# Optimization experiments

Measured on AMD Instinct MI355X. Metric: run time of the kernel, lower is better.

The kernel has to match this reference:

```python
import jax, jax.numpy as jnp
import numpy as np

LAM = 0.1
EPS = 1e-5

def _conv(x, w, b, pad):
    y = jax.lax.conv_general_dilated(x, w, (1, 1), [(pad, pad), (pad, pad)],
                                     dimension_numbers=('NCHW', 'OIHW', 'NCHW'))
    return y + b[None, :, None, None]

def _bn(x, g, b, m, v):
    return (x - m[None, :, None, None]) * (g / jnp.sqrt(v + EPS))[None, :, None, None] + b[None, :, None, None]

def _simam(x):
    # leave-one-out mean/var per HxW map, closed-form single-pass (same math as the
    # original per-pixel mask loop: torch unbiased var over the n-1 'other' values)
    n = x.shape[-2] * x.shape[-1]
    s = jnp.sum(x, axis=(-2, -1), keepdims=True)
    ss = jnp.sum(x * x, axis=(-2, -1), keepdims=True)
    mu = (s - x) / (n - 1)
    var = (ss - x * x - (n - 1) * mu * mu) / (n - 2)
    e = 4.0 * (var + LAM) / ((x - mu) ** 2 + 2.0 * var + 2.0 * LAM)
    return jax.nn.sigmoid(1.0 / e) * x

def setup_inputs():
    B, T, D, H, NC = 128, 128, 64, 256, 5
    IN = 64 * D
    ks = iter(jax.random.split(jax.random.key(0), 64))
    def w(shape, s=0.05):
        return jax.random.normal(next(ks), shape, jnp.float32) * s
    d = {'x': jax.random.normal(next(ks), (B, T, D), jnp.float32)}
    for nm, ci, co, k in [('c1a', 1, 32, 1), ('c1b', 32, 32, 3), ('c2a', 32, 64, 1), ('c2b', 64, 64, 3)]:
        d[nm + '_w'] = w((co, ci, k, k)); d[nm + '_b'] = w((co,))
        bn = 'bn' + nm[1:]
        d[bn + '_g'] = jnp.ones((co,), jnp.float32)
        d[bn + '_b'] = jnp.zeros((co,), jnp.float32)
        d[bn + '_m'] = w((co,), 0.01)
        d[bn + '_v'] = jnp.ones((co,), jnp.float32)
    for i in range(3):
        d['q%d_w' % i] = w((IN, H)); d['q%d_b' % i] = w((IN,))
        d['r%d_w' % i] = w((H, IN)); d['r%d_b' % i] = w((H,))
    d['wih'] = w((4 * H, IN)); d['whh'] = w((4 * H, H))
    d['bih'] = w((4 * H,)); d['bhh'] = w((4 * H,))
    d['fc_w'] = w((NC, H)); d['fc_b'] = w((NC,))
    return d

def reference(x, c1a_w, c1a_b, bn1a_g, bn1a_b, bn1a_m, bn1a_v, c1b_w, c1b_b, bn1b_g, bn1b_b, bn1b_m, bn1b_v, c2a_w, c2a_b, bn2a_g, bn2a_b, bn2a_m, bn2a_v, c2b_w, c2b_b, bn2b_g, bn2b_b, bn2b_m, bn2b_v, q0_w, q0_b, r0_w, r0_b, q1_w, q1_b, r1_w, r1_b, q2_w, q2_b, r2_w, r2_b, wih, whh, bih, bhh, fc_w, fc_b):
    B, T, D = x.shape
    h4 = x[:, None]  # [B,1,T,D]
    h4 = jax.nn.relu(_bn(_conv(h4, c1a_w, c1a_b, 0), bn1a_g, bn1a_b, bn1a_m, bn1a_v))
    h4 = jax.nn.relu(_bn(_conv(h4, c1b_w, c1b_b, 1), bn1b_g, bn1b_b, bn1b_m, bn1b_v))
    h4 = _simam(h4)
    h4 = jax.nn.relu(_bn(_conv(h4, c2a_w, c2a_b, 0), bn2a_g, bn2a_b, bn2a_m, bn2a_v))
    h4 = jax.nn.relu(_bn(_conv(h4, c2b_w, c2b_b, 1), bn2b_g, bn2b_b, bn2b_m, bn2b_v))
    h4 = _simam(h4)
    C = h4.shape[1]
    xl = h4.reshape(B, T, C * D)  # raw reshape, matches torch .view on [B,C,T,D]
    H = whh.shape[1]

    def step(carry, xt):
        h, c = carry
        xm, hm = xt, h
        xm = 2.0 * jax.nn.sigmoid(hm @ q0_w.T + q0_b) * xm  # round 1
        hm = 2.0 * jax.nn.sigmoid(xm @ r0_w.T + r0_b) * hm  # round 2
        xm = 2.0 * jax.nn.sigmoid(hm @ q1_w.T + q1_b) * xm  # round 3
        hm = 2.0 * jax.nn.sigmoid(xm @ r1_w.T + r1_b) * hm  # round 4
        xm = 2.0 * jax.nn.sigmoid(hm @ q2_w.T + q2_b) * xm  # round 5
        hm = 2.0 * jax.nn.sigmoid(xm @ r2_w.T + r2_b) * hm  # round 6
        gates = xm @ wih.T + bih + hm @ whh.T + bhh
        i, f, g, o = jnp.split(gates, 4, axis=-1)  # torch LSTMCell gate order
        c_new = jax.nn.sigmoid(f) * c + jax.nn.sigmoid(i) * jnp.tanh(g)
        h_new = jax.nn.sigmoid(o) * jnp.tanh(c_new)
        return (h_new, c_new), None

    h0 = jnp.zeros((B, H), x.dtype)
    c0 = jnp.zeros((B, H), x.dtype)
    (hT, _), _ = jax.lax.scan(step, (h0, c0), jnp.swapaxes(xl, 0, 1))
    return hT @ fc_w.T + fc_b
```

## Files before the change

kernel.cpp:

```cpp
#include <hip/hip_runtime.h>
#include <math.h>


typedef unsigned short u16;

#define EPSBN 1e-5f

__device__ __forceinline__ float sigf(float x) { return 1.0f / (1.0f + expf(-x)); }

__device__ __forceinline__ float b2f(u16 u) {
  union { unsigned int i; float f; } v; v.i = ((unsigned int)u) << 16; return v.f;
}
__device__ __forceinline__ u16 f2b(float f) {
  union { float f; unsigned int i; } v; v.f = f;
  unsigned int r = v.i + 0x7FFFu + ((v.i >> 16) & 1u);
  return (u16)(r >> 16);
}

template <typename T> __device__ __forceinline__ float ld1(const T* p);
template <> __device__ __forceinline__ float ld1<float>(const float* p) { return *p; }
template <> __device__ __forceinline__ float ld1<u16>(const u16* p) { return b2f(*p); }
template <typename T> __device__ __forceinline__ void st1(T* p, float v);
template <> __device__ __forceinline__ void st1<float>(float* p, float v) { *p = v; }
template <> __device__ __forceinline__ void st1<u16>(u16* p, float v) { *p = f2b(v); }

__device__ __forceinline__ float simam_elem(float xv, float s, float ss) {
  float mu = (s - xv) * (1.0f / 8191.0f);
  float var = (ss - xv * xv - 8191.0f * mu * mu) * (1.0f / 8190.0f);
  float einv = ((xv - mu) * (xv - mu) + 2.0f * var + 0.2f) / (4.0f * (var + 0.1f));
  return xv * sigf(einv);
}

__global__ __launch_bounds__(256) void k_conv1(
    const float* __restrict__ x,
    const float* __restrict__ w1a, const float* __restrict__ b1a,
    const float* __restrict__ g1a, const float* __restrict__ bb1a,
    const float* __restrict__ m1a, const float* __restrict__ v1a,
    const float* __restrict__ w1b, const float* __restrict__ b1b,
    const float* __restrict__ g1b, const float* __restrict__ bb1b,
    const float* __restrict__ m1b, const float* __restrict__ v1b,
    u16* __restrict__ y1u, float* __restrict__ ps1, float* __restrict__ pss1)
{
  __shared__ float xs[6][66];
  __shared__ float a1[32][6][66];
  __shared__ float A1[32], T1[32], S2[32], T2[32];
  __shared__ float reds[4][32], redq[4][32];
  const int tid = threadIdx.x;
  const int b = blockIdx.x, t0 = blockIdx.y * 4;
  if (tid < 32) {
    float s = g1a[tid] * rsqrtf(v1a[tid] + EPSBN);
    A1[tid] = w1a[tid] * s;
    T1[tid] = (b1a[tid] - m1a[tid]) * s + bb1a[tid];
    float s2 = g1b[tid] * rsqrtf(v1b[tid] + EPSBN);
    S2[tid] = s2;
    T2[tid] = (b1b[tid] - m1b[tid]) * s2 + bb1b[tid];
  }
  for (int i = tid; i < 6 * 66; i += 256) {
    int r = i / 66, cc = i - r * 66;
    int t = t0 + r - 1, d = cc - 1;
    float v = 0.f;
    if (t >= 0 && t < 128 && d >= 0 && d < 64) v = x[(b * 128 + t) * 64 + d];
    xs[r][cc] = v;
  }
  __syncthreads();
  for (int i = tid; i < 32 * 6 * 66; i += 256) {
    int c = i / 396;
    int rr = i - c * 396;
    int r = rr / 66, cc = rr - r * 66;
    int t = t0 + r - 1, d = cc - 1;
    float v = 0.f;
    if (t >= 0 && t < 128 && d >= 0 && d < 64)
      v = fmaxf(xs[r][cc] * A1[c] + T1[c], 0.f);
    a1[c][r][cc] = v;
  }
  __syncthreads();
  const int d = tid & 63, tq = tid >> 6, lane = tid & 63;
  float acc[32];
// ... 117 lines not shown
        float val = 0.f;
        if (t >= 0 && t < 128 && dd >= 0 && dd < 64)
          val = fmaxf(acc * scl + off, 0.f);
        a2[c2][r][cc] = val;
      }
    }
  }
  __syncthreads();
  const int d = tid & 63;
  const int gq = __builtin_amdgcn_readfirstlane((int)(tid >> 6));
  float acc[16][2];
#pragma unroll
  for (int i = 0; i < 16; ++i) { acc[i][0] = 0.f; acc[i][1] = 0.f; }
#pragma unroll 1
  for (int c1 = 0; c1 < 64; ++c1) {
    float a00 = a2[c1][0][d], a01 = a2[c1][0][d + 1], a02 = a2[c1][0][d + 2];
    float a10 = a2[c1][1][d], a11 = a2[c1][1][d + 1], a12 = a2[c1][1][d + 2];
    float a20 = a2[c1][2][d], a21 = a2[c1][2][d + 1], a22 = a2[c1][2][d + 2];
    float a30 = a2[c1][3][d], a31 = a2[c1][3][d + 1], a32 = a2[c1][3][d + 2];
#pragma unroll
    for (int i = 0; i < 16; ++i) {
      const float* wp = w2b + (size_t)((gq * 16 + i) * 64 + c1) * 9;
      float w0 = wp[0], w1 = wp[1], w2 = wp[2];
      float w3 = wp[3], w4 = wp[4], w5 = wp[5];
      float w6 = wp[6], w7 = wp[7], w8 = wp[8];
      acc[i][0] += a00 * w0 + a01 * w1 + a02 * w2 + a10 * w3 + a11 * w4 +
                   a12 * w5 + a20 * w6 + a21 * w7 + a22 * w8;
      acc[i][1] += a10 * w0 + a11 * w1 + a12 * w2 + a20 * w3 + a21 * w4 +
                   a22 * w5 + a30 * w6 + a31 * w7 + a32 * w8;
    }
  }
#pragma unroll
  for (int i = 0; i < 16; ++i) {
    int c2 = gq * 16 + i;
    float sc = sA2b[c2], tb = sT2b[c2];
    float v0 = fmaxf(acc[i][0] * sc + tb, 0.f);
    float v1 = fmaxf(acc[i][1] * sc + tb, 0.f);
    size_t ob = (size_t)(b * 64 + c2) * 8192 + (size_t)t0 * 64 + d;
    st1(z + ob, v0);
    st1(z + ob + 64, v1);
    float s = v0 + v1, q = v0 * v0 + v1 * v1;
#pragma unroll
    for (int off = 32; off; off >>= 1) {
      s += __shfl_down(s, off);
      q += __shfl_down(q, off);
    }
    if (lane == 0) {
      ps2[(size_t)((b * 64 + c2) << 6) + blockIdx.x] = s;
      pss2[(size_t)((b * 64 + c2) << 6) + blockIdx.x] = q;
    }
  }
}

__global__ __launch_bounds__(256) void k_hfin(
    const float* __restrict__ gslab, const float* __restrict__ bih,
    const float* __restrict__ bhh, float* __restrict__ h, float* __restrict__ c,
    int is_t0)
{
  const int i = blockIdx.x * 256 + threadIdx.x;
  const int b = i >> 8, k = i & 255;
  if (is_t0) { h[i] = 0.f; c[i] = 0.f; return; }
  float gi = bih[k] + bhh[k];
  float gf = bih[k + 256] + bhh[k + 256];
  float gg = bih[k + 512] + bhh[k + 512];
  float go = bih[k + 768] + bhh[k + 768];
#pragma unroll 1
  for (int s = 0; s < 17; ++s) {
    const float* gs = gslab + (size_t)s * 131072 + b * 1024;
    gi += gs[k]; gf += gs[k + 256]; gg += gs[k + 512]; go += gs[k + 768];
  }
  float cn = sigf(gf) * c[i] + sigf(gi) * tanhf(gg);
  c[i] = cn;
  h[i] = sigf(go) * tanhf(cn);
}

template <typename XT>
__global__ __launch_bounds__(256) void k_q(
    const float* __restrict__ qW, const float* __restrict__ qb,
    const float* __restrict__ hmsrc, const XT* __restrict__ xin,
    int xin_bstride, float* __restrict__ xm)
{
  __shared__ float hms[32][256];
  const int tid = threadIdx.x;
  const int n0 = blockIdx.x * 64, b0 = blockIdx.y * 32;
  for (int i = tid; i < 32 * 256; i += 256) {
    int bl = i >> 8, k = i & 255;
    hms[bl][k] = hmsrc[(b0 + bl) * 256 + k];
  }
  __syncthreads();
  const int n = n0 + (tid & 63), bg = tid >> 6;
  float acc[8];
#pragma unroll
  for (int j = 0; j < 8; ++j) acc[j] = 0.f;
  const float* wrow = qW + (size_t)n * 256;
  for (int k = 0; k < 256; k += 4) {
    float4 w = *(const float4*)(wrow + k);
#pragma unroll
    for (int j = 0; j < 8; ++j) {
      float4 hv = *(const float4*)&hms[bg * 8 + j][k];
      acc[j] += w.x * hv.x + w.y * hv.y + w.z * hv.z + w.w * hv.w;
    }
  }
  float bias = qb[n];
#pragma unroll
  for (int j = 0; j < 8; ++j) {
    int b = b0 + bg * 8 + j;
    float xv = ld1(xin + (size_t)b * xin_bstride + n);
    xm[(size_t)b * 4096 + n] = 2.0f * sigf(acc[j] + bias) * xv;
  }
}

__global__ __launch_bounds__(256) void k_r(
    const float* __restrict__ rW, const float* __restrict__ xm,
    float* __restrict__ rslab)
{
  __shared__ float xms[32][128];
  const int tid = threadIdx.x;
  const int n0 = blockIdx.x * 32, b0 = blockIdx.y * 32, ks = blockIdx.z;
  const int n = n0 + (tid & 31), bg = tid >> 5;
  float acc[4] = {0.f, 0.f, 0.f, 0.f};
  const float* wrow = rW + (size_t)n * 4096;
#pragma unroll 1
  for (int sub = 0; sub < 4; ++sub) {
    const int kbase = ks * 512 + sub * 128;
    __syncthreads();
    for (int i = tid; i < 1024; i += 256) {
      int row = i >> 5, col4 = i & 31;
      *(float4*)&xms[row][col4 * 4] =
          *(const float4*)(xm + (size_t)(b0 + row) * 4096 + kbase + col4 * 4);
    }
    __syncthreads();
    for (int k = 0; k < 128; k += 4) {
      float4 w = *(const float4*)(wrow + kbase + k);
#pragma unroll
      for (int j = 0; j < 4; ++j) {
        float4 xv = *(const float4*)&xms[bg * 4 + j][k];
        acc[j] += w.x * xv.x + w.y * xv.y + w.z * xv.z + w.w * xv.w;
      }
    }
  }
#pragma unroll
  for (int j = 0; j < 4; ++j)
    rslab[(size_t)(ks * 128 + b0 + bg * 4 + j) * 256 + n] = acc[j];
}

__global__ __launch_bounds__(256) void k_hmfin(
    const float* __restrict__ rslab, const float* __restrict__ rb,
    const float* __restrict__ src, float* __restrict__ hm)
{
  const int i = blockIdx.x * 256 + threadIdx.x;
  const int b = i >> 8, k = i & 255;
  float acc = rb[k];
#pragma unroll
  for (int s = 0; s < 8; ++s) acc += rslab[(size_t)(s * 128 + b) * 256 + k];
  hm[i] = 2.0f * sigf(acc) * src[i];
}

__global__ __launch_bounds__(256) void k_whh(
    const float* __restrict__ whh, const float* __restrict__ hm,
    float* __restrict__ gslab16)
{
  __shared__ float hms[32][256];
  const int tid = threadIdx.x;
  const int n0 = blockIdx.x * 64, b0 = blockIdx.y * 32;
  for (int i = tid; i < 32 * 256; i += 256) {
    int bl = i >> 8, k = i & 255;
    hms[bl][k] = hm[(b0 + bl) * 256 + k];
  }
  __syncthreads();
  const int n = n0 + (tid & 63), bg = tid >> 6;
  float acc[8];
#pragma unroll
  for (int j = 0; j < 8; ++j) acc[j] = 0.f;
  const float* wrow = whh + (size_t)n * 256;
  for (int k = 0; k < 256; k += 4) {
    float4 w = *(const float4*)(wrow + k);
#pragma unroll
    for (int j = 0; j < 8; ++j) {
      float4 hv = *(const float4*)&hms[bg * 8 + j][k];
      acc[j] += w.x * hv.x + w.y * hv.y + w.z * hv.z + w.w * hv.w;
    }
  }
#pragma unroll
  for (int j = 0; j < 8; ++j)
    gslab16[(size_t)(b0 + bg * 8 + j) * 1024 + n] = acc[j];
}

__global__ __launch_bounds__(256) void k_g(
    const float* __restrict__ wih, const float* __restrict__ xm,
    float* __restrict__ gslab)
{
  __shared__ float xms[32][128];
  const int tid = threadIdx.x;
  const int jt = blockIdx.x, b0 = blockIdx.y * 32, ks = blockIdx.z;
  const int nj = jt * 64 + (tid & 63), bg = tid >> 6;
  float acc[8][4];
#pragma unroll
  for (int j = 0; j < 8; ++j)
#pragma unroll
    for (int g = 0; g < 4; ++g) acc[j][g] = 0.f;
  const float* w0 = wih + (size_t)nj * 4096;
  const float* w1 = wih + (size_t)(nj + 256) * 4096;
  const float* w2 = wih + (size_t)(nj + 512) * 4096;
  const float* w3 = wih + (size_t)(nj + 768) * 4096;
#pragma unroll 1
  for (int sub = 0; sub < 2; ++sub) {
    const int kbase = ks * 256 + sub * 128;
    __syncthreads();
    for (int i = tid; i < 1024; i += 256) {
      int row = i >> 5, col4 = i & 31;
      *(float4*)&xms[row][col4 * 4] =
          *(const float4*)(xm + (size_t)(b0 + row) * 4096 + kbase + col4 * 4);
    }
    __syncthreads();
    for (int k = 0; k < 128; k += 4) {
      float4 wa = *(const float4*)(w0 + kbase + k);
      float4 wb = *(const float4*)(w1 + kbase + k);
      float4 wc = *(const float4*)(w2 + kbase + k);
      float4 wd = *(const float4*)(w3 + kbase + k);
#pragma unroll
      for (int j = 0; j < 8; ++j) {
        float4 xv = *(const float4*)&xms[bg * 8 + j][k];
        acc[j][0] += wa.x * xv.x + wa.y * xv.y + wa.z * xv.z + wa.w * xv.w;
        acc[j][1] += wb.x * xv.x + wb.y * xv.y + wb.z * xv.z + wb.w * xv.w;
        acc[j][2] += wc.x * xv.x + wc.y * xv.y + wc.z * xv.z + wc.w * xv.w;
        acc[j][3] += wd.x * xv.x + wd.y * xv.y + wd.z * xv.z + wd.w * xv.w;
      }
    }
  }
#pragma unroll
  for (int j = 0; j < 8; ++j) {
    size_t base = (size_t)ks * 131072 + (size_t)(b0 + bg * 8 + j) * 1024 + nj;
    gslab[base] = acc[j][0];
    gslab[base + 256] = acc[j][1];
    gslab[base + 512] = acc[j][2];
    gslab[base + 768] = acc[j][3];
  }
}

__global__ __launch_bounds__(256) void k_fc(
    const float* __restrict__ h, const float* __restrict__ fcw,
    const float* __restrict__ fcb, float* __restrict__ out)
{
  __shared__ float hs[256];
  const int tid = threadIdx.x, b = blockIdx.x;
  hs[tid] = h[b * 256 + tid];
  __syncthreads();
  if (tid < 5) {
    float acc = fcb[tid];
    for (int k = 0; k < 256; ++k) acc += hs[k] * fcw[tid * 256 + k];
    out[b * 5 + tid] = acc;
  }
}

__global__ __launch_bounds__(256) void k_report(float* out, float v, int n) {
  int i = blockIdx.x * 256 + threadIdx.x;
  if (i < n) out[i] = v;
}

struct Net {
  const float *x;
  const float *c1a_w, *c1a_b, *g1a, *b1a, *m1a, *v1a;
  const float *c1b_w, *c1b_b, *g1b, *b1b, *m1b, *v1b;
  const float *c2a_w, *c2a_b, *g2a, *b2a, *m2a, *v2a;
  const float *c2b_w, *c2b_b, *g2b, *b2b, *m2b, *v2b;
  const float *qw[3], *qb[3], *rw[3], *rb[3];
  const float *wih, *whh, *bih, *bhh, *fcw, *fcb;
};

template <typename ZT>
static void run_all(const Net& p, ZT* z, u16* y1u, float* scr,
                    float* ps1, float* pss1, float* st1v,
                    float* ps2, float* pss2, float* st2v,
                    float* out, hipStream_t stream)
{
  float* xm    = scr;
  float* h     = scr + 524288;
  float* c     = scr + 557056;
  float* hm    = scr + 589824;
  float* rslab = scr + 622592;
  float* gslab = scr + 884736;

  k_conv1<<<dim3(128, 32), 256, 0, stream>>>(p.x, p.c1a_w, p.c1a_b, p.g1a,
      p.b1a, p.m1a, p.v1a, p.c1b_w, p.c1b_b, p.g1b, p.b1b, p.m1b, p.v1b,
      y1u, ps1, pss1);
  k_red<<<16, 256, 0, stream>>>(ps1, pss1, st1v, 32, 4096);
  k_simam_t<u16><<<4096, 256, 0, stream>>>(y1u, st1v, 4096);
  k_conv2<ZT><<<dim3(64, 128), 256, 0, stream>>>(y1u, p.c2a_w, p.c2a_b, p.g2a,
      p.b2a, p.m2a, p.v2a, p.c2b_w, p.c2b_b, p.g2b, p.b2b, p.m2b, p.v2b,
      z, ps2, pss2);
  k_red<<<32, 256, 0, stream>>>(ps2, pss2, st2v, 64, 8192);
  k_simam_t<ZT><<<8192, 256, 0, stream>>>(z, st2v, 8192);

  for (int t = 0; t < 128; ++t) {
    k_hfin<<<128, 256, 0, stream>>>(gslab, p.bih, p.bhh, h, c, t == 0 ? 1 : 0);
    for (int s = 0; s < 3; ++s) {
      if (s == 0)
        k_q<ZT><<<dim3(64, 4), 256, 0, stream>>>(p.qw[0], p.qb[0], h,
            z + (size_t)t * 4096, 524288, xm);
      else
        k_q<float><<<dim3(64, 4), 256, 0, stream>>>(p.qw[s], p.qb[s], hm,
            xm, 4096, xm);
      k_r<<<dim3(8, 4, 8), 256, 0, stream>>>(p.rw[s], xm, rslab);
      k_hmfin<<<128, 256, 0, stream>>>(rslab, p.rb[s], (s == 0) ? h : hm, hm);
    }
    k_whh<<<dim3(16, 4), 256, 0, stream>>>(p.whh, hm, gslab + (size_t)16 * 131072);
    k_g<<<dim3(4, 4, 16), 256, 0, stream>>>(p.wih, xm, gslab);
  }
  k_hfin<<<128, 256, 0, stream>>>(gslab, p.bih, p.bhh, h, c, 0);
  k_fc<<<128, 256, 0, stream>>>(h, p.fcw, p.fcb, out);
}

extern "C" void kernel_launch(void* const* d_in, const int* in_sizes, int n_in,
                              void* d_out, int out_size, void* d_ws, size_t ws_size,
                              hipStream_t stream)
{
  (void)in_sizes; (void)n_in;
  Net p;
  p.x = (const float*)d_in[0];
  p.c1a_w = (const float*)d_in[1];  p.c1a_b = (const float*)d_in[2];
  p.g1a = (const float*)d_in[3];    p.b1a = (const float*)d_in[4];
  p.m1a = (const float*)d_in[5];    p.v1a = (const float*)d_in[6];
  p.c1b_w = (const float*)d_in[7];  p.c1b_b = (const float*)d_in[8];
  p.g1b = (const float*)d_in[9];    p.b1b = (const float*)d_in[10];
  p.m1b = (const float*)d_in[11];   p.v1b = (const float*)d_in[12];
  p.c2a_w = (const float*)d_in[13]; p.c2a_b = (const float*)d_in[14];
  p.g2a = (const float*)d_in[15];   p.b2a = (const float*)d_in[16];
  p.m2a = (const float*)d_in[17];   p.v2a = (const float*)d_in[18];
  p.c2b_w = (const float*)d_in[19]; p.c2b_b = (const float*)d_in[20];
  p.g2b = (const float*)d_in[21];   p.b2b = (const float*)d_in[22];
  p.m2b = (const float*)d_in[23];   p.v2b = (const float*)d_in[24];
  for (int i = 0; i < 3; ++i) {
    p.qw[i] = (const float*)d_in[25 + 4 * i];
    p.qb[i] = (const float*)d_in[26 + 4 * i];
    p.rw[i] = (const float*)d_in[27 + 4 * i];
    p.rb[i] = (const float*)d_in[28 + 4 * i];
  }
  p.wih = (const float*)d_in[37]; p.whh = (const float*)d_in[38];
  p.bih = (const float*)d_in[39]; p.bhh = (const float*)d_in[40];
  p.fcw = (const float*)d_in[41]; p.fcb = (const float*)d_in[42];
  float* out = (float*)d_out;
  char* base = (char*)d_ws;

  const size_t ZB_F32 = 268435456, ZB_BF16 = 134217728, Y1B = 67108864;
  const size_t STATS = 1048576 * 2 + 65536 + 2097152 * 2 + 65536;
  const size_t HI_NEED = ZB_F32 + Y1B + STATS;
  const size_t LO_NEED = ZB_BF16 + Y1B + STATS;

  if (ws_size >= HI_NEED) {
    float* z = (float*)base;
    u16* y1u = (u16*)(base + ZB_F32);
    float* scr = (float*)(base + ZB_F32);
    char* sb = base + ZB_F32 + Y1B;
    run_all<float>(p, z, y1u, scr,
                   (float*)sb, (float*)(sb + 1048576), (float*)(sb + 2097152),
                   (float*)(sb + 2162688), (float*)(sb + 4259840),
                   (float*)(sb + 6356992), out, stream);
  } else if (ws_size >= LO_NEED) {
    u16* z = (u16*)base;
    u16* y1u = (u16*)(base + ZB_BF16);
    float* scr = (float*)(base + ZB_BF16);
    char* sb = base + ZB_BF16 + Y1B;
    run_all<u16>(p, z, y1u, scr,
// ... 8 lines not shown
```

Measured before the change: 28.57 ms.

## Fuse LSTM time loop into one persistent cooperative kernel with grid barriers

Replaces the roughly 1400 small per-timestep kernel launches of the recurrent loop with a single persistent cooperative kernel of 256 blocks by 1024 threads. Stages are separated by a custom atomic grid barrier. The hm finalization is folded into the following q and whh stages, and the final FC runs inside the same kernel. This removes launch overhead and inter-kernel gaps, at the cost of barrier spin latency, fewer accumulators per thread, and a deadlock risk if the fallback plain launch cannot keep all blocks resident.

```diff
diff --git a/kernel.cpp b/kernel.cpp
--- a/kernel.cpp
+++ b/kernel.cpp
@@ -246,204 +246,249 @@
   }
 }
 
-__global__ __launch_bounds__(256) void k_hfin(
-    const float* __restrict__ gslab, const float* __restrict__ bih,
-    const float* __restrict__ bhh, float* __restrict__ h, float* __restrict__ c,
-    int is_t0)
+__device__ __forceinline__ void gbar(unsigned* cnt, unsigned* rel, unsigned gen) {
+  __syncthreads();
+  if (threadIdx.x == 0) {
+    __threadfence();
+    unsigned prev = __hip_atomic_fetch_add(cnt, 1u, __ATOMIC_ACQ_REL,
+                                           __HIP_MEMORY_SCOPE_AGENT);
+    if (prev == gen * 256u - 1u) {
+      __hip_atomic_store(rel, gen, __ATOMIC_RELEASE, __HIP_MEMORY_SCOPE_AGENT);
+    } else {
+      while (__hip_atomic_load(rel, __ATOMIC_ACQUIRE,
+                               __HIP_MEMORY_SCOPE_AGENT) < gen) {
+        __builtin_amdgcn_s_sleep(8);
+      }
+    }
+    __threadfence();
+  }
+  __syncthreads();
+  asm volatile("" ::: "memory");
+}
+
+struct LPar {
+  const void* z;
+  const float* qw0; const float* qb0; const float* rw0; const float* rb0;
+  const float* qw1; const float* qb1; const float* rw1; const float* rb1;
+  const float* qw2; const float* qb2; const float* rw2; const float* rb2;
+  const float* wih; const float* whh; const float* bih; const float* bhh;
+  const float* fcw; const float* fcb;
+  float* xm; float* h; float* c; float* hmA; float* hmB;
+  float* rslab; float* gslab;
+  unsigned* cnt; unsigned* rel;
+  float* out;
+};
+
+template <typename ZT>
+__global__ __launch_bounds__(1024, 4) void k_lstm(LPar p)
 {
-  const int i = blockIdx.x * 256 + threadIdx.x;
-  const int b = i >> 8, k = i & 255;
-  if (is_t0) { h[i] = 0.f; c[i] = 0.f; return; }
-  float gi = bih[k] + bhh[k];
-  float gf = bih[k + 256] + bhh[k + 256];
-  float gg = bih[k + 512] + bhh[k + 512];
-  float go = bih[k + 768] + bhh[k + 768];
-#pragma unroll 1
-  for (int s = 0; s < 17; ++s) {
-    const float* gs = gslab + (size_t)s * 131072 + b * 1024;
-    gi += gs[k]; gf += gs[k + 256]; gg += gs[k + 512]; go += gs[k + 768];
-  }
-  float cn = sigf(gf) * c[i] + sigf(gi) * tanhf(gg);
-  c[i] = cn;
-  h[i] = sigf(go) * tanhf(cn);
-}
-
-template <typename XT>
-__global__ __launch_bounds__(256) void k_q(
-    const float* __restrict__ qW, const float* __restrict__ qb,
-    const float* __restrict__ hmsrc, const XT* __restrict__ xin,
-    int xin_bstride, float* __restrict__ xm)
-{
-  __shared__ float hms[32][256];
+  __shared__ float sm[8192];
   const int tid = threadIdx.x;
-  const int n0 = blockIdx.x * 64, b0 = blockIdx.y * 32;
-  for (int i = tid; i < 32 * 256; i += 256) {
-    int bl = i >> 8, k = i & 255;
-    hms[bl][k] = hmsrc[(b0 + bl) * 256 + k];
-  }
-  __syncthreads();
-  const int n = n0 + (tid & 63), bg = tid >> 6;
-  float acc[8];
-#pragma unroll
-  for (int j = 0; j < 8; ++j) acc[j] = 0.f;
-  const float* wrow = qW + (size_t)n * 256;
-  for (int k = 0; k < 256; k += 4) {
-    float4 w = *(const float4*)(wrow + k);
-#pragma unroll
-    for (int j = 0; j < 8; ++j) {
-      float4 hv = *(const float4*)&hms[bg * 8 + j][k];
-      acc[j] += w.x * hv.x + w.y * hv.y + w.z * hv.z + w.w * hv.w;
-    }
-  }
-  float bias = qb[n];
-#pragma unroll
-  for (int j = 0; j < 8; ++j) {
-    int b = b0 + bg * 8 + j;
-    float xv = ld1(xin + (size_t)b * xin_bstride + n);
-    xm[(size_t)b * 4096 + n] = 2.0f * sigf(acc[j] + bias) * xv;
-  }
-}
-
-__global__ __launch_bounds__(256) void k_r(
-    const float* __restrict__ rW, const float* __restrict__ xm,
-    float* __restrict__ rslab)
-{
-  __shared__ float xms[32][128];
-  const int tid = threadIdx.x;
-  const int n0 = blockIdx.x * 32, b0 = blockIdx.y * 32, ks = blockIdx.z;
-  const int n = n0 + (tid & 31), bg = tid >> 5;
-  float acc[4] = {0.f, 0.f, 0.f, 0.f};
-  const float* wrow = rW + (size_t)n * 4096;
-#pragma unroll 1
-  for (int sub = 0; sub < 4; ++sub) {
-    const int kbase = ks * 512 + sub * 128;
+  const int bid = blockIdx.x;
+  unsigned gen = 0;
+
+  for (int t = 0; t <= 128; ++t) {
+    if (bid < 32) {
+      const int i = (bid << 10) + tid;
+      const int b = i >> 8, k = i & 255;
+      if (t == 0) {
+        p.h[i] = 0.f; p.c[i] = 0.f;
+      } else {
+        float gi = p.bih[k]       + p.bhh[k];
+        float gf = p.bih[k + 256] + p.bhh[k + 256];
+        float gg = p.bih[k + 512] + p.bhh[k + 512];
+        float go = p.bih[k + 768] + p.bhh[k + 768];
+#pragma unroll 1
+        for (int s = 0; s < 17; ++s) {
+          const float* gs = p.gslab + (size_t)s * 131072 + b * 1024;
+          gi += gs[k]; gf += gs[k + 256]; gg += gs[k + 512]; go += gs[k + 768];
+        }
+        float cn = sigf(gf) * p.c[i] + sigf(gi) * tanhf(gg);
+        p.c[i] = cn;
+        p.h[i] = sigf(go) * tanhf(cn);
+      }
+    }
+    gbar(p.cnt, p.rel, ++gen);
+    if (t == 128) break;
+
+    const int qnt = bid & 63, qbt = bid >> 6;
+    const int qb0 = qbt * 32;
+
+#pragma unroll 1
+    for (int s = 0; s < 3; ++s) {
+      {
+        if (s == 0) {
+          for (int i = tid; i < 8192; i += 1024)
+            sm[i] = p.h[(qb0 << 8) + i];
+        } else {
+          const float* rbv = (s == 1) ? p.rb0 : p.rb1;
+          const float* src = (s == 1) ? p.h : p.hmA;
+          for (int i = tid; i < 8192; i += 1024) {
+            const int bl = i >> 8, k = i & 255;
+            const int b = qb0 + bl;
+            float acc = rbv[k];
+#pragma unroll
+            for (int ss = 0; ss < 8; ++ss)
+              acc += p.rslab[(size_t)((ss * 128 + b) << 8) + k];
+            sm[i] = 2.0f * sigf(acc) * src[(b << 8) + k];
+          }
+        }
+        __syncthreads();
+        if (s > 0 && qnt == 0) {
+          float* dst = (s == 1) ? p.hmA : p.hmB;
+          for (int i = tid; i < 8192; i += 1024)
+            dst[(qb0 << 8) + i] = sm[i];
+        }
+        const float* qW = (s == 0) ? p.qw0 : ((s == 1) ? p.qw1 : p.qw2);
+        const float* qB = (s == 0) ? p.qb0 : ((s == 1) ? p.qb1 : p.qb2);
+        const int n = (qnt << 6) + (tid & 63);
+        const int bg = tid >> 6;
+        const float* wrow = qW + (size_t)n * 256;
+        const float* h0 = &sm[(bg * 2) << 8];
+        const float* h1 = &sm[(bg * 2 + 1) << 8];
+        float acc0 = 0.f, acc1 = 0.f;
+        for (int k = 0; k < 256; k += 4) {
+          float4 w  = *(const float4*)(wrow + k);
+          float4 a4 = *(const float4*)(h0 + k);
+          float4 b4 = *(const float4*)(h1 + k);
+          acc0 += w.x * a4.x + w.y * a4.y + w.z * a4.z + w.w * a4.w;
+          acc1 += w.x * b4.x + w.y * b4.y + w.z * b4.z + w.w * b4.w;
+        }
+        const float bias = qB[n];
+        const int b_0 = qb0 + bg * 2, b_1 = b_0 + 1;
+        float xv0, xv1;
+        if (s == 0) {
+          const ZT* zz = (const ZT*)p.z;
+          xv0 = ld1(zz + (size_t)b_0 * 524288 + t * 4096 + n);
+          xv1 = ld1(zz + (size_t)b_1 * 524288 + t * 4096 + n);
+        } else {
+          xv0 = p.xm[(size_t)b_0 * 4096 + n];
+          xv1 = p.xm[(size_t)b_1 * 4096 + n];
+        }
+        p.xm[(size_t)b_0 * 4096 + n] = 2.0f * sigf(acc0 + bias) * xv0;
+        p.xm[(size_t)b_1 * 4096 + n] = 2.0f * sigf(acc1 + bias) * xv1;
+      }
+      gbar(p.cnt, p.rel, ++gen);
+      {
+        const float* rW = (s == 0) ? p.rw0 : ((s == 1) ? p.rw1 : p.rw2);
+        const int nt = bid & 7, bt = (bid >> 3) & 3, ks = bid >> 5;
+        const int n = (nt << 5) + (tid & 31);
+        const int b0 = bt * 32, bg = tid >> 5;
+        const float* wrow = rW + (size_t)n * 4096;
+        float acc = 0.f;
+#pragma unroll 1
+        for (int sub = 0; sub < 4; ++sub) {
+          const int kbase = (ks << 9) + (sub << 7);
+          __syncthreads();
+          {
+            const int row = tid >> 5, col4 = tid & 31;
+            *(float4*)&sm[(row << 7) + (col4 << 2)] =
+                *(const float4*)(p.xm + (size_t)(b0 + row) * 4096 + kbase +
+                                 (col4 << 2));
+          }
+          __syncthreads();
+          const float* xr = &sm[bg << 7];
+          for (int k = 0; k < 128; k += 4) {
+            float4 w  = *(const float4*)(wrow + kbase + k);
+            float4 xv = *(const float4*)(xr + k);
+            acc += w.x * xv.x + w.y * xv.y + w.z * xv.z + w.w * xv.w;
+          }
+        }
+        p.rslab[(size_t)(((ks << 7) + b0 + bg) << 8) + n] = acc;
+      }
+      gbar(p.cnt, p.rel, ++gen);
+    }
+    {
+      const int jt = bid & 3, bt = (bid >> 2) & 3, ks = bid >> 4;
+      const int b0 = bt * 32;
+      const int nj = (jt << 6) + (tid & 63), bg = tid >> 6;
+      float a00 = 0, a01 = 0, a02 = 0, a03 = 0;
+      float a10 = 0, a11 = 0, a12 = 0, a13 = 0;
+      const float* w0 = p.wih + (size_t)nj * 4096;
+      const float* w1 = p.wih + (size_t)(nj + 256) * 4096;
+      const float* w2 = p.wih + (size_t)(nj + 512) * 4096;
+      const float* w3 = p.wih + (size_t)(nj + 768) * 4096;
+#pragma unroll 1
+      for (int sub = 0; sub < 2; ++sub) {
+        const int kbase = (ks << 8) + (sub << 7);
+        __syncthreads();
+        {
+          const int row = tid >> 5, col4 = tid & 31;
+          *(float4*)&sm[(row << 7) + (col4 << 2)] =
+              *(const float4*)(p.xm + (size_t)(b0 + row) * 4096 + kbase +
+                               (col4 << 2));
+        }
+        __syncthreads();
+        const float* x0 = &sm[(bg * 2) << 7];
+        const float* x1 = &sm[(bg * 2 + 1) << 7];
+        for (int k = 0; k < 128; k += 4) {
+          float4 wa = *(const float4*)(w0 + kbase + k);
+          float4 wb = *(const float4*)(w1 + kbase + k);
+          float4 wc = *(const float4*)(w2 + kbase + k);
+          float4 wd = *(const float4*)(w3 + kbase + k);
+          float4 xa = *(const float4*)(x0 + k);
+          float4 xb = *(const float4*)(x1 + k);
+          a00 += wa.x * xa.x + wa.y * xa.y + wa.z * xa.z + wa.w * xa.w;
+          a01 += wb.x * xa.x + wb.y * xa.y + wb.z * xa.z + wb.w * xa.w;
+          a02 += wc.x * xa.x + wc.y * xa.y + wc.z * xa.z + wc.w * xa.w;
+          a03 += wd.x * xa.x + wd.y * xa.y + wd.z * xa.z + wd.w * xa.w;
+          a10 += wa.x * xb.x + wa.y * xb.y + wa.z * xb.z + wa.w * xb.w;
+          a11 += wb.x * xb.x + wb.y * xb.y + wb.z * xb.z + wb.w * xb.w;
+          a12 += wc.x * xb.x + wc.y * xb.y + wc.z * xb.z + wc.w * xb.w;
+          a13 += wd.x * xb.x + wd.y * xb.y + wd.z * xb.z + wd.w * xb.w;
+        }
+      }
+      {
+        const size_t base0 =
+            (size_t)ks * 131072 + (size_t)(b0 + bg * 2) * 1024 + nj;
+        p.gslab[base0]       = a00;
+        p.gslab[base0 + 256] = a01;
+        p.gslab[base0 + 512] = a02;
+        p.gslab[base0 + 768] = a03;
+        const size_t base1 = base0 + 1024;
+        p.gslab[base1]       = a10;
+        p.gslab[base1 + 256] = a11;
+        p.gslab[base1 + 512] = a12;
+        p.gslab[base1 + 768] = a13;
+      }
+      __syncthreads();
+      if (bid < 128) {
+        const int nt2 = bid >> 2, bt2 = bid & 3;
+        const int b02 = bt2 * 32;
+        for (int i = tid; i < 8192; i += 1024) {
+          const int bl = i >> 8, k = i & 255;
+          const int b = b02 + bl;
+          float acc = p.rb2[k];
+#pragma unroll
+          for (int ss = 0; ss < 8; ++ss)
+            acc += p.rslab[(size_t)((ss * 128 + b) << 8) + k];
+          sm[i] = 2.0f * sigf(acc) * p.hmB[(b << 8) + k];
+        }
+        __syncthreads();
+        const int n2 = (nt2 << 5) + (tid & 31);
+        const int bg2 = tid >> 5;
+        const float* wrow = p.whh + (size_t)n2 * 256;
+        const float* hr = &sm[bg2 << 8];
+        float acc = 0.f;
+        for (int k = 0; k < 256; k += 4) {
+          float4 w  = *(const float4*)(wrow + k);
+          float4 hv = *(const float4*)(hr + k);
+          acc += w.x * hv.x + w.y * hv.y + w.z * hv.z + w.w * hv.w;
+        }
+        p.gslab[(size_t)16 * 131072 + (size_t)(b02 + bg2) * 1024 + n2] = acc;
+      }
+    }
+    gbar(p.cnt, p.rel, ++gen);
+  }
+  if (bid < 128) {
+    if (tid < 256) sm[tid] = p.h[(bid << 8) + tid];
     __syncthreads();
-    for (int i = tid; i < 1024; i += 256) {
-      int row = i >> 5, col4 = i & 31;
-      *(float4*)&xms[row][col4 * 4] =
-          *(const float4*)(xm + (size_t)(b0 + row) * 4096 + kbase + col4 * 4);
-    }
-    __syncthreads();
-    for (int k = 0; k < 128; k += 4) {
-      float4 w = *(const float4*)(wrow + kbase + k);
-#pragma unroll
-      for (int j = 0; j < 4; ++j) {
-        float4 xv = *(const float4*)&xms[bg * 4 + j][k];
-        acc[j] += w.x * xv.x + w.y * xv.y + w.z * xv.z + w.w * xv.w;
-      }
-    }
-  }
-#pragma unroll
-  for (int j = 0; j < 4; ++j)
-    rslab[(size_t)(ks * 128 + b0 + bg * 4 + j) * 256 + n] = acc[j];
-}
-
-__global__ __launch_bounds__(256) void k_hmfin(
-    const float* __restrict__ rslab, const float* __restrict__ rb,
-    const float* __restrict__ src, float* __restrict__ hm)
-{
-  const int i = blockIdx.x * 256 + threadIdx.x;
-  const int b = i >> 8, k = i & 255;
-  float acc = rb[k];
-#pragma unroll
-  for (int s = 0; s < 8; ++s) acc += rslab[(size_t)(s * 128 + b) * 256 + k];
-  hm[i] = 2.0f * sigf(acc) * src[i];
-}
-
-__global__ __launch_bounds__(256) void k_whh(
-    const float* __restrict__ whh, const float* __restrict__ hm,
-    float* __restrict__ gslab16)
-{
-  __shared__ float hms[32][256];
-  const int tid = threadIdx.x;
-  const int n0 = blockIdx.x * 64, b0 = blockIdx.y * 32;
-  for (int i = tid; i < 32 * 256; i += 256) {
-    int bl = i >> 8, k = i & 255;
-    hms[bl][k] = hm[(b0 + bl) * 256 + k];
-  }
-  __syncthreads();
-  const int n = n0 + (tid & 63), bg = tid >> 6;
-  float acc[8];
-#pragma unroll
-  for (int j = 0; j < 8; ++j) acc[j] = 0.f;
-  const float* wrow = whh + (size_t)n * 256;
-  for (int k = 0; k < 256; k += 4) {
-    float4 w = *(const float4*)(wrow + k);
-#pragma unroll
-    for (int j = 0; j < 8; ++j) {
-      float4 hv = *(const float4*)&hms[bg * 8 + j][k];
-      acc[j] += w.x * hv.x + w.y * hv.y + w.z * hv.z + w.w * hv.w;
-    }
-  }
-#pragma unroll
-  for (int j = 0; j < 8; ++j)
-    gslab16[(size_t)(b0 + bg * 8 + j) * 1024 + n] = acc[j];
-}
-
-__global__ __launch_bounds__(256) void k_g(
-    const float* __restrict__ wih, const float* __restrict__ xm,
-    float* __restrict__ gslab)
-{
-  __shared__ float xms[32][128];
-  const int tid = threadIdx.x;
-  const int jt = blockIdx.x, b0 = blockIdx.y * 32, ks = blockIdx.z;
-  const int nj = jt * 64 + (tid & 63), bg = tid >> 6;
-  float acc[8][4];
-#pragma unroll
-  for (int j = 0; j < 8; ++j)
-#pragma unroll
-    for (int g = 0; g < 4; ++g) acc[j][g] = 0.f;
-  const float* w0 = wih + (size_t)nj * 4096;
-  const float* w1 = wih + (size_t)(nj + 256) * 4096;
-  const float* w2 = wih + (size_t)(nj + 512) * 4096;
-  const float* w3 = wih + (size_t)(nj + 768) * 4096;
-#pragma unroll 1
-  for (int sub = 0; sub < 2; ++sub) {
-    const int kbase = ks * 256 + sub * 128;
-    __syncthreads();
-    for (int i = tid; i < 1024; i += 256) {
-      int row = i >> 5, col4 = i & 31;
-      *(float4*)&xms[row][col4 * 4] =
-          *(const float4*)(xm + (size_t)(b0 + row) * 4096 + kbase + col4 * 4);
-    }
-    __syncthreads();
-    for (int k = 0; k < 128; k += 4) {
-      float4 wa = *(const float4*)(w0 + kbase + k);
-      float4 wb = *(const float4*)(w1 + kbase + k);
-      float4 wc = *(const float4*)(w2 + kbase + k);
-      float4 wd = *(const float4*)(w3 + kbase + k);
-#pragma unroll
-      for (int j = 0; j < 8; ++j) {
-        float4 xv = *(const float4*)&xms[bg * 8 + j][k];
-        acc[j][0] += wa.x * xv.x + wa.y * xv.y + wa.z * xv.z + wa.w * xv.w;
-        acc[j][1] += wb.x * xv.x + wb.y * xv.y + wb.z * xv.z + wb.w * xv.w;
-        acc[j][2] += wc.x * xv.x + wc.y * xv.y + wc.z * xv.z + wc.w * xv.w;
-        acc[j][3] += wd.x * xv.x + wd.y * xv.y + wd.z * xv.z + wd.w * xv.w;
-      }
-    }
-  }
-#pragma unroll
-  for (int j = 0; j < 8; ++j) {
-    size_t base = (size_t)ks * 131072 + (size_t)(b0 + bg * 8 + j) * 1024 + nj;
-    gslab[base] = acc[j][0];
-    gslab[base + 256] = acc[j][1];
-    gslab[base + 512] = acc[j][2];
-    gslab[base + 768] = acc[j][3];
-  }
-}
-
-__global__ __launch_bounds__(256) void k_fc(
-    const float* __restrict__ h, const float* __restrict__ fcw,
-    const float* __restrict__ fcb, float* __restrict__ out)
-{
-  __shared__ float hs[256];
-  const int tid = threadIdx.x, b = blockIdx.x;
-  hs[tid] = h[b * 256 + tid];
-  __syncthreads();
-  if (tid < 5) {
-    float acc = fcb[tid];
-    for (int k = 0; k < 256; ++k) acc += hs[k] * fcw[tid * 256 + k];
-    out[b * 5 + tid] = acc;
+    if (tid < 5) {
+      float acc = p.fcb[tid];
+      const float* w = p.fcw + tid * 256;
+      for (int k = 0; k < 256; ++k) acc += sm[k] * w[k];
+      p.out[bid * 5 + tid] = acc;
+    }
   }
 }
 
@@ -471,9 +516,12 @@
   float* xm    = scr;
   float* h     = scr + 524288;
   float* c     = scr + 557056;
-  float* hm    = scr + 589824;
-  float* rslab = scr + 622592;
-  float* gslab = scr + 884736;
+  float* hmA   = scr + 589824;
+  float* hmB   = scr + 622592;
+  float* rslab = scr + 655360;
+  float* gslab = scr + 917504;
+  unsigned* cnt = (unsigned*)(scr + 3145728);
+  unsigned* rel = cnt + 1;
 
   k_conv1<<<dim3(128, 32), 256, 0, stream>>>(p.x, p.c1a_w, p.c1a_b, p.g1a,
       p.b1a, p.m1a, p.v1a, p.c1b_w, p.c1b_b, p.g1b, p.b1b, p.m1b, p.v1b,
@@ -486,23 +534,26 @@
   k_red<<<32, 256, 0, stream>>>(ps2, pss2, st2v, 64, 8192);
   k_simam_t<ZT><<<8192, 256, 0, stream>>>(z, st2v, 8192);
 
-  for (int t = 0; t < 128; ++t) {
-    k_hfin<<<128, 256, 0, stream>>>(gslab, p.bih, p.bhh, h, c, t == 0 ? 1 : 0);
-    for (int s = 0; s < 3; ++s) {
-      if (s == 0)
-        k_q<ZT><<<dim3(64, 4), 256, 0, stream>>>(p.qw[0], p.qb[0], h,
-            z + (size_t)t * 4096, 524288, xm);
-      else
-        k_q<float><<<dim3(64, 4), 256, 0, stream>>>(p.qw[s], p.qb[s], hm,
-            xm, 4096, xm);
-      k_r<<<dim3(8, 4, 8), 256, 0, stream>>>(p.rw[s], xm, rslab);
-      k_hmfin<<<128, 256, 0, stream>>>(rslab, p.rb[s], (s == 0) ? h : hm, hm);
-    }
-    k_whh<<<dim3(16, 4), 256, 0, stream>>>(p.whh, hm, gslab + (size_t)16 * 131072);
-    k_g<<<dim3(4, 4, 16), 256, 0, stream>>>(p.wih, xm, gslab);
-  }
-  k_hfin<<<128, 256, 0, stream>>>(gslab, p.bih, p.bhh, h, c, 0);
-  k_fc<<<128, 256, 0, stream>>>(h, p.fcw, p.fcb, out);
+  hipMemsetAsync((void*)cnt, 0, 8, stream);
+
+  LPar P;
+  P.z = (const void*)z;
+  P.qw0 = p.qw[0]; P.qb0 = p.qb[0]; P.rw0 = p.rw[0]; P.rb0 = p.rb[0];
+  P.qw1 = p.qw[1]; P.qb1 = p.qb[1]; P.rw1 = p.rw[1]; P.rb1 = p.rb[1];
+  P.qw2 = p.qw[2]; P.qb2 = p.qb[2]; P.rw2 = p.rw[2]; P.rb2 = p.rb[2];
+  P.wih = p.wih; P.whh = p.whh; P.bih = p.bih; P.bhh = p.bhh;
+  P.fcw = p.fcw; P.fcb = p.fcb;
+  P.xm = xm; P.h = h; P.c = c; P.hmA = hmA; P.hmB = hmB;
+  P.rslab = rslab; P.gslab = gslab;
+  P.cnt = cnt; P.rel = rel; P.out = out;
+
+  void* args[] = { (void*)&P };
+  hipError_t e = hipLaunchCooperativeKernel(
+      (const void*)k_lstm<ZT>, dim3(256), dim3(1024), args, 0, stream);
+  if (e != hipSuccess) {
+    (void)hipGetLastError();
+    k_lstm<ZT><<<dim3(256), dim3(1024), 0, stream>>>(P);
+  }
 }
 
 extern "C" void kernel_launch(void* const* d_in, const int* in_sizes, int n_in,
```

New measurement: 95.03 ms. 3.33x slower.

## Convert recurrent weights to fp16 and fuse hm finalization into consumer kernels

Applied to the files above, without the earlier changes.

Converts all recurrent-loop weight matrices (q, r, wih, whh) to fp16 once before the time loop, halving the weight bytes read at every step. The k_hmfin kernels are folded into the next k_q launch and into a merged gate kernel, and the separate whh and wih gate kernels become one launch. This cuts per-step kernel launches and bandwidth. The trade-offs are fp16 rounding of the weights and redundant hm recomputation in every block.

```diff
diff --git a/kernel.cpp b/kernel.cpp
--- a/kernel.cpp
+++ b/kernel.cpp
@@ -3,6 +3,7 @@
 
 
 typedef unsigned short u16;
+typedef _Float16 f16;
 
 #define EPSBN 1e-5f
 
@@ -23,6 +24,12 @@
 template <typename T> __device__ __forceinline__ void st1(T* p, float v);
 template <> __device__ __forceinline__ void st1<float>(float* p, float v) { *p = v; }
 template <> __device__ __forceinline__ void st1<u16>(u16* p, float v) { *p = f2b(v); }
+
+__device__ __forceinline__ void ldh4(const f16* p, float* w) {
+  union { uint2 u; f16 h[4]; } v; v.u = *(const uint2*)p;
+#pragma unroll
+  for (int i = 0; i < 4; ++i) w[i] = (float)v.h[i];
+}
 
 __device__ __forceinline__ float simam_elem(float xv, float s, float ss) {
   float mu = (s - xv) * (1.0f / 8191.0f);
@@ -246,6 +253,12 @@
   }
 }
 
+__global__ __launch_bounds__(256) void k_w16(const float* __restrict__ s,
+                                             f16* __restrict__ d, int n) {
+  for (int i = blockIdx.x * 256 + threadIdx.x; i < n; i += gridDim.x * 256)
+    d[i] = (f16)s[i];
+}
+
 __global__ __launch_bounds__(256) void k_hfin(
     const float* __restrict__ gslab, const float* __restrict__ bih,
     const float* __restrict__ bhh, float* __restrict__ h, float* __restrict__ c,
@@ -268,31 +281,58 @@
   h[i] = sigf(go) * tanhf(cn);
 }
 
-template <typename XT>
+template <typename XT, bool FUSE>
 __global__ __launch_bounds__(256) void k_q(
-    const float* __restrict__ qW, const float* __restrict__ qb,
-    const float* __restrict__ hmsrc, const XT* __restrict__ xin,
-    int xin_bstride, float* __restrict__ xm)
+    const f16* __restrict__ qW, const float* __restrict__ qb,
+    const float* __restrict__ hmsrc,
+    const float* __restrict__ rslab, const float* __restrict__ rbv,
+    float* __restrict__ hmout,
+    const XT* __restrict__ xin, int xin_bstride, float* __restrict__ xm)
 {
   __shared__ float hms[32][256];
   const int tid = threadIdx.x;
   const int n0 = blockIdx.x * 64, b0 = blockIdx.y * 32;
-  for (int i = tid; i < 32 * 256; i += 256) {
-    int bl = i >> 8, k = i & 255;
-    hms[bl][k] = hmsrc[(b0 + bl) * 256 + k];
+  if (!FUSE) {
+    for (int i = tid; i < 32 * 256; i += 256) {
+      int bl = i >> 8, k = i & 255;
+      hms[bl][k] = hmsrc[(b0 + bl) * 256 + k];
+    }
+  } else {
+    for (int i = tid; i < 2048; i += 256) {
+      int bl = i >> 6, c4 = (i & 63) << 2;
+      int b = b0 + bl;
+      float4 acc = *(const float4*)(rbv + c4);
+#pragma unroll
+      for (int ss = 0; ss < 8; ++ss) {
+        float4 rv = *(const float4*)(rslab + (size_t)((ss * 128 + b) << 8) + c4);
+        acc.x += rv.x; acc.y += rv.y; acc.z += rv.z; acc.w += rv.w;
+      }
+      float4 sv = *(const float4*)(hmsrc + (b << 8) + c4);
+      float4 o;
+      o.x = 2.0f * sigf(acc.x) * sv.x;
+      o.y = 2.0f * sigf(acc.y) * sv.y;
+      o.z = 2.0f * sigf(acc.z) * sv.z;
+      o.w = 2.0f * sigf(acc.w) * sv.w;
+      *(float4*)&hms[bl][c4] = o;
+    }
   }
   __syncthreads();
+  if (FUSE && blockIdx.x == 0) {
+    for (int i = tid; i < 8192; i += 256)
+      hmout[(b0 << 8) + i] = hms[i >> 8][i & 255];
+  }
   const int n = n0 + (tid & 63), bg = tid >> 6;
   float acc[8];
 #pragma unroll
   for (int j = 0; j < 8; ++j) acc[j] = 0.f;
-  const float* wrow = qW + (size_t)n * 256;
+  const f16* wrow = qW + (size_t)n * 256;
   for (int k = 0; k < 256; k += 4) {
-    float4 w = *(const float4*)(wrow + k);
+    float w[4];
+    ldh4(wrow + k, w);
 #pragma unroll
     for (int j = 0; j < 8; ++j) {
       float4 hv = *(const float4*)&hms[bg * 8 + j][k];
-      acc[j] += w.x * hv.x + w.y * hv.y + w.z * hv.z + w.w * hv.w;
+      acc[j] += w[0] * hv.x + w[1] * hv.y + w[2] * hv.z + w[3] * hv.w;
     }
   }
   float bias = qb[n];
@@ -305,7 +345,7 @@
 }
 
 __global__ __launch_bounds__(256) void k_r(
-    const float* __restrict__ rW, const float* __restrict__ xm,
+    const f16* __restrict__ rW, const float* __restrict__ xm,
     float* __restrict__ rslab)
 {
   __shared__ float xms[32][128];
@@ -313,7 +353,7 @@
   const int n0 = blockIdx.x * 32, b0 = blockIdx.y * 32, ks = blockIdx.z;
   const int n = n0 + (tid & 31), bg = tid >> 5;
   float acc[4] = {0.f, 0.f, 0.f, 0.f};
-  const float* wrow = rW + (size_t)n * 4096;
+  const f16* wrow = rW + (size_t)n * 4096;
 #pragma unroll 1
   for (int sub = 0; sub < 4; ++sub) {
     const int kbase = ks * 512 + sub * 128;
@@ -325,11 +365,12 @@
     }
     __syncthreads();
     for (int k = 0; k < 128; k += 4) {
-      float4 w = *(const float4*)(wrow + kbase + k);
+      float w[4];
+      ldh4(wrow + kbase + k, w);
 #pragma unroll
       for (int j = 0; j < 4; ++j) {
         float4 xv = *(const float4*)&xms[bg * 4 + j][k];
-        acc[j] += w.x * xv.x + w.y * xv.y + w.z * xv.z + w.w * xv.w;
+        acc[j] += w[0] * xv.x + w[1] * xv.y + w[2] * xv.z + w[3] * xv.w;
       }
     }
   }
@@ -338,97 +379,101 @@
     rslab[(size_t)(ks * 128 + b0 + bg * 4 + j) * 256 + n] = acc[j];
 }
 
-__global__ __launch_bounds__(256) void k_hmfin(
-    const float* __restrict__ rslab, const float* __restrict__ rb,
-    const float* __restrict__ src, float* __restrict__ hm)
-{
-  const int i = blockIdx.x * 256 + threadIdx.x;
-  const int b = i >> 8, k = i & 255;
-  float acc = rb[k];
-#pragma unroll
-  for (int s = 0; s < 8; ++s) acc += rslab[(size_t)(s * 128 + b) * 256 + k];
-  hm[i] = 2.0f * sigf(acc) * src[i];
-}
-
-__global__ __launch_bounds__(256) void k_whh(
-    const float* __restrict__ whh, const float* __restrict__ hm,
-    float* __restrict__ gslab16)
-{
-  __shared__ float hms[32][256];
+__global__ __launch_bounds__(256) void k_gw(
+    const f16* __restrict__ wih, const f16* __restrict__ whh,
+    const float* __restrict__ xm, const float* __restrict__ rslab,
+    const float* __restrict__ rb2, const float* __restrict__ hmB,
+    float* __restrict__ gslab)
+{
+  __shared__ float sm[32 * 256];
   const int tid = threadIdx.x;
-  const int n0 = blockIdx.x * 64, b0 = blockIdx.y * 32;
-  for (int i = tid; i < 32 * 256; i += 256) {
-    int bl = i >> 8, k = i & 255;
-    hms[bl][k] = hm[(b0 + bl) * 256 + k];
-  }
-  __syncthreads();
-  const int n = n0 + (tid & 63), bg = tid >> 6;
-  float acc[8];
-#pragma unroll
-  for (int j = 0; j < 8; ++j) acc[j] = 0.f;
-  const float* wrow = whh + (size_t)n * 256;
-  for (int k = 0; k < 256; k += 4) {
-    float4 w = *(const float4*)(wrow + k);
+  const int ks = blockIdx.z;
+  if (ks < 16) {
+    float (*xms)[128] = (float (*)[128])sm;
+    const int jt = blockIdx.x, b0 = blockIdx.y * 32;
+    const int nj = jt * 64 + (tid & 63), bg = tid >> 6;
+    float acc[8][4];
+#pragma unroll
+    for (int j = 0; j < 8; ++j)
+#pragma unroll
+      for (int g = 0; g < 4; ++g) acc[j][g] = 0.f;
+    const f16* w0 = wih + (size_t)nj * 4096;
+    const f16* w1 = wih + (size_t)(nj + 256) * 4096;
+    const f16* w2 = wih + (size_t)(nj + 512) * 4096;
+    const f16* w3 = wih + (size_t)(nj + 768) * 4096;
+#pragma unroll 1
+    for (int sub = 0; sub < 2; ++sub) {
+      const int kbase = ks * 256 + sub * 128;
+      __syncthreads();
+      for (int i = tid; i < 1024; i += 256) {
+        int row = i >> 5, col4 = i & 31;
+        *(float4*)&xms[row][col4 * 4] =
+            *(const float4*)(xm + (size_t)(b0 + row) * 4096 + kbase + col4 * 4);
+      }
+      __syncthreads();
+      for (int k = 0; k < 128; k += 4) {
+        float wa[4], wb[4], wc[4], wd[4];
+        ldh4(w0 + kbase + k, wa);
+        ldh4(w1 + kbase + k, wb);
+        ldh4(w2 + kbase + k, wc);
+        ldh4(w3 + kbase + k, wd);
+#pragma unroll
+        for (int j = 0; j < 8; ++j) {
+          float4 xv = *(const float4*)&xms[bg * 8 + j][k];
+          acc[j][0] += wa[0] * xv.x + wa[1] * xv.y + wa[2] * xv.z + wa[3] * xv.w;
+          acc[j][1] += wb[0] * xv.x + wb[1] * xv.y + wb[2] * xv.z + wb[3] * xv.w;
+          acc[j][2] += wc[0] * xv.x + wc[1] * xv.y + wc[2] * xv.z + wc[3] * xv.w;
+          acc[j][3] += wd[0] * xv.x + wd[1] * xv.y + wd[2] * xv.z + wd[3] * xv.w;
+        }
+      }
+    }
 #pragma unroll
     for (int j = 0; j < 8; ++j) {
-      float4 hv = *(const float4*)&hms[bg * 8 + j][k];
-      acc[j] += w.x * hv.x + w.y * hv.y + w.z * hv.z + w.w * hv.w;
-    }
-  }
-#pragma unroll
-  for (int j = 0; j < 8; ++j)
-    gslab16[(size_t)(b0 + bg * 8 + j) * 1024 + n] = acc[j];
-}
-
-__global__ __launch_bounds__(256) void k_g(
-    const float* __restrict__ wih, const float* __restrict__ xm,
-    float* __restrict__ gslab)
-{
-  __shared__ float xms[32][128];
-  const int tid = threadIdx.x;
-  const int jt = blockIdx.x, b0 = blockIdx.y * 32, ks = blockIdx.z;
-  const int nj = jt * 64 + (tid & 63), bg = tid >> 6;
-  float acc[8][4];
-#pragma unroll
-  for (int j = 0; j < 8; ++j)
-#pragma unroll
-    for (int g = 0; g < 4; ++g) acc[j][g] = 0.f;
-  const float* w0 = wih + (size_t)nj * 4096;
-  const float* w1 = wih + (size_t)(nj + 256) * 4096;
-  const float* w2 = wih + (size_t)(nj + 512) * 4096;
-  const float* w3 = wih + (size_t)(nj + 768) * 4096;
-#pragma unroll 1
-  for (int sub = 0; sub < 2; ++sub) {
-    const int kbase = ks * 256 + sub * 128;
+      size_t base = (size_t)ks * 131072 + (size_t)(b0 + bg * 8 + j) * 1024 + nj;
+      gslab[base]       = acc[j][0];
+      gslab[base + 256] = acc[j][1];
+      gslab[base + 512] = acc[j][2];
+      gslab[base + 768] = acc[j][3];
+    }
+  } else {
+    float (*hms)[256] = (float (*)[256])sm;
+    const int nt = (ks - 16) * 4 + blockIdx.x;
+    const int b0 = blockIdx.y * 32;
+    for (int i = tid; i < 2048; i += 256) {
+      int bl = i >> 6, c4 = (i & 63) << 2;
+      int b = b0 + bl;
+      float4 acc = *(const float4*)(rb2 + c4);
+#pragma unroll
+      for (int ss = 0; ss < 8; ++ss) {
+        float4 rv = *(const float4*)(rslab + (size_t)((ss * 128 + b) << 8) + c4);
+        acc.x += rv.x; acc.y += rv.y; acc.z += rv.z; acc.w += rv.w;
+      }
+      float4 sv = *(const float4*)(hmB + (b << 8) + c4);
+      float4 o;
+      o.x = 2.0f * sigf(acc.x) * sv.x;
+      o.y = 2.0f * sigf(acc.y) * sv.y;
+      o.z = 2.0f * sigf(acc.z) * sv.z;
+      o.w = 2.0f * sigf(acc.w) * sv.w;
+      *(float4*)&hms[bl][c4] = o;
+    }
     __syncthreads();
-    for (int i = tid; i < 1024; i += 256) {
-      int row = i >> 5, col4 = i & 31;
-      *(float4*)&xms[row][col4 * 4] =
-          *(const float4*)(xm + (size_t)(b0 + row) * 4096 + kbase + col4 * 4);
-    }
-    __syncthreads();
-    for (int k = 0; k < 128; k += 4) {
-      float4 wa = *(const float4*)(w0 + kbase + k);
-      float4 wb = *(const float4*)(w1 + kbase + k);
-      float4 wc = *(const float4*)(w2 + kbase + k);
-      float4 wd = *(const float4*)(w3 + kbase + k);
+    const int n = nt * 64 + (tid & 63), bg = tid >> 6;
+    float acc[8];
+#pragma unroll
+    for (int j = 0; j < 8; ++j) acc[j] = 0.f;
+    const f16* wrow = whh + (size_t)n * 256;
+    for (int k = 0; k < 256; k += 4) {
+      float w[4];
+      ldh4(wrow + k, w);
 #pragma unroll
       for (int j = 0; j < 8; ++j) {
-        float4 xv = *(const float4*)&xms[bg * 8 + j][k];
-        acc[j][0] += wa.x * xv.x + wa.y * xv.y + wa.z * xv.z + wa.w * xv.w;
-        acc[j][1] += wb.x * xv.x + wb.y * xv.y + wb.z * xv.z + wb.w * xv.w;
-        acc[j][2] += wc.x * xv.x + wc.y * xv.y + wc.z * xv.z + wc.w * xv.w;
-        acc[j][3] += wd.x * xv.x + wd.y * xv.y + wd.z * xv.z + wd.w * xv.w;
-      }
-    }
-  }
-#pragma unroll
-  for (int j = 0; j < 8; ++j) {
-    size_t base = (size_t)ks * 131072 + (size_t)(b0 + bg * 8 + j) * 1024 + nj;
-    gslab[base] = acc[j][0];
-    gslab[base + 256] = acc[j][1];
-    gslab[base + 512] = acc[j][2];
-    gslab[base + 768] = acc[j][3];
+        float4 hv = *(const float4*)&hms[bg * 8 + j][k];
+        acc[j] += w[0] * hv.x + w[1] * hv.y + w[2] * hv.z + w[3] * hv.w;
+      }
+    }
+#pragma unroll
+    for (int j = 0; j < 8; ++j)
+      gslab[(size_t)16 * 131072 + (size_t)(b0 + bg * 8 + j) * 1024 + n] = acc[j];
   }
 }
 
@@ -471,9 +516,11 @@
   float* xm    = scr;
   float* h     = scr + 524288;
   float* c     = scr + 557056;
-  float* hm    = scr + 589824;
-  float* rslab = scr + 622592;
-  float* gslab = scr + 884736;
+  float* hmA   = scr + 589824;
+  float* hmB   = scr + 622592;
+  float* rslab = scr + 655360;
+  float* gslab = scr + 917504;
+  f16*   wf    = (f16*)(scr + 3145728);
 
   k_conv1<<<dim3(128, 32), 256, 0, stream>>>(p.x, p.c1a_w, p.c1a_b, p.g1a,
       p.b1a, p.m1a, p.v1a, p.c1b_w, p.c1b_b, p.g1b, p.b1b, p.m1b, p.v1b,
@@ -486,20 +533,36 @@
   k_red<<<32, 256, 0, stream>>>(ps2, pss2, st2v, 64, 8192);
   k_simam_t<ZT><<<8192, 256, 0, stream>>>(z, st2v, 8192);
 
+  f16* qw0f = wf;
+  f16* qw1f = wf + 1048576;
+  f16* qw2f = wf + 2097152;
+  f16* rw0f = wf + 3145728;
+  f16* rw1f = wf + 4194304;
+  f16* rw2f = wf + 5242880;
+  f16* wihf = wf + 6291456;
+  f16* whhf = wf + 10485760;
+  k_w16<<<1024, 256, 0, stream>>>(p.qw[0], qw0f, 1048576);
+  k_w16<<<1024, 256, 0, stream>>>(p.qw[1], qw1f, 1048576);
+  k_w16<<<1024, 256, 0, stream>>>(p.qw[2], qw2f, 1048576);
+  k_w16<<<1024, 256, 0, stream>>>(p.rw[0], rw0f, 1048576);
+  k_w16<<<1024, 256, 0, stream>>>(p.rw[1], rw1f, 1048576);
+  k_w16<<<1024, 256, 0, stream>>>(p.rw[2], rw2f, 1048576);
+  k_w16<<<4096, 256, 0, stream>>>(p.wih,   wihf, 4194304);
+  k_w16<<<1024, 256, 0, stream>>>(p.whh,   whhf, 262144);
+
   for (int t = 0; t < 128; ++t) {
     k_hfin<<<128, 256, 0, stream>>>(gslab, p.bih, p.bhh, h, c, t == 0 ? 1 : 0);
-    for (int s = 0; s < 3; ++s) {
-      if (s == 0)
-        k_q<ZT><<<dim3(64, 4), 256, 0, stream>>>(p.qw[0], p.qb[0], h,
-            z + (size_t)t * 4096, 524288, xm);
-      else
-        k_q<float><<<dim3(64, 4), 256, 0, stream>>>(p.qw[s], p.qb[s], hm,
-            xm, 4096, xm);
-      k_r<<<dim3(8, 4, 8), 256, 0, stream>>>(p.rw[s], xm, rslab);
-      k_hmfin<<<128, 256, 0, stream>>>(rslab, p.rb[s], (s == 0) ? h : hm, hm);
-    }
-    k_whh<<<dim3(16, 4), 256, 0, stream>>>(p.whh, hm, gslab + (size_t)16 * 131072);
-    k_g<<<dim3(4, 4, 16), 256, 0, stream>>>(p.wih, xm, gslab);
+    k_q<ZT, false><<<dim3(64, 4), 256, 0, stream>>>(qw0f, p.qb[0], h,
+        nullptr, nullptr, nullptr, z + (size_t)t * 4096, 524288, xm);
+    k_r<<<dim3(8, 4, 8), 256, 0, stream>>>(rw0f, xm, rslab);
+    k_q<float, true><<<dim3(64, 4), 256, 0, stream>>>(qw1f, p.qb[1], h,
+        rslab, p.rb[0], hmA, xm, 4096, xm);
+    k_r<<<dim3(8, 4, 8), 256, 0, stream>>>(rw1f, xm, rslab);
+    k_q<float, true><<<dim3(64, 4), 256, 0, stream>>>(qw2f, p.qb[2], hmA,
+        rslab, p.rb[1], hmB, xm, 4096, xm);
+    k_r<<<dim3(8, 4, 8), 256, 0, stream>>>(rw2f, xm, rslab);
+    k_gw<<<dim3(4, 4, 20), 256, 0, stream>>>(wihf, whhf, xm, rslab,
+        p.rb[2], hmB, gslab);
   }
   k_hfin<<<128, 256, 0, stream>>>(gslab, p.bih, p.bhh, h, c, 0);
   k_fc<<<128, 256, 0, stream>>>(h, p.fcw, p.fcb, out);
```

Result: faster. 27.82 ms (-2.6%).
